# Kernel tuning notes

Measured on AMD Instinct MI355X. Metric: run time of the kernel, lower is better.

Reference implementation:

```python
import jax, jax.numpy as jnp
import numpy as np

N, D, R, E = 50000, 256, 4, 800000
LN_EPS = 1e-5
NEG_INF = -1e30  # finite stand-in for -inf so softmax stays grad-safe


def _layernorm(x, g, b):
    m = x.mean(axis=-1, keepdims=True)
    v = x.var(axis=-1, keepdims=True)
    return (x - m) / jnp.sqrt(v + LN_EPS) * g + b


def setup_inputs() -> dict:
    key = jax.random.key(0)
    ks = jax.random.split(key, 8)
    s = 1.0 / np.sqrt(D).astype(np.float32)
    return {
        'rows': jax.random.randint(ks[0], (R, E), 0, N),
        'cols': jax.random.randint(ks[1], (R, E), 0, N),
        'vals': jax.random.uniform(ks[2], (R, E), jnp.float32),
        'node_emb': jax.random.normal(ks[3], (N, D), jnp.float32) * s,
        'pre_W': jax.random.normal(ks[4], (D, D), jnp.float32) * s,
        'pre_b': jnp.zeros((D,), jnp.float32),
        'ln1_g': jnp.ones((D,), jnp.float32),
        'ln1_b': jnp.zeros((D,), jnp.float32),
        'rel_W': jax.random.normal(ks[5], (R, D, D), jnp.float32) * s,
        'attn_vec': jax.random.normal(ks[6], (D,), jnp.float32) * s,
        'self_W': jax.random.normal(ks[7], (D, D), jnp.float32) * s,
        'self_b': jnp.zeros((D,), jnp.float32),
        'bias': jnp.zeros((D,), jnp.float32),
        'ln2_g': jnp.ones((D,), jnp.float32),
        'ln2_b': jnp.zeros((D,), jnp.float32),
    }


def reference(rows, cols, vals, node_emb, pre_W, pre_b, ln1_g, ln1_b, rel_W,
              attn_vec, self_W, self_b, bias, ln2_g, ln2_b):
    # active_indices = arange(N), so x_all is the full embedding table
    x_all = node_emb
    # pre_encoder: Linear -> LayerNorm -> GELU (exact erf, torch default)
    x = jax.nn.gelu(_layernorm(x_all @ pre_W + pre_b, ln1_g, ln1_b), approximate=False)
    # per-relation: relation linear then SpMM (adj_t @ x_rel) via gather + segment_sum
    msgs = []
    for i in range(R):
        x_rel = x @ rel_W[i]                              # [N, D]
        contrib = vals[i][:, None] * x_rel[cols[i]]       # [E, D]
        msgs.append(jax.ops.segment_sum(contrib, rows[i], num_segments=N))
    stacked = jnp.stack(msgs, axis=1)                     # [N, R, D]
    # semantic attention over relations
    scores = jnp.einsum('nrd,d->nr', stacked, attn_vec)   # [N, R]
    mask = jnp.any(stacked != 0, axis=2)                  # [N, R]
    attn = jax.nn.softmax(jnp.where(mask, scores, NEG_INF), axis=1)
    attn = attn * mask                                    # == nan_to_num(softmax(-inf rows))
    out = jnp.einsum('nrd,nr->nd', stacked, attn) + bias + (x @ self_W + self_b)
    out = jax.nn.gelu(out, approximate=False)
    # active_indices = arange(N): scatter into global index space is identity
    final = _layernorm(out, ln2_g, ln2_b)
    return final, attn, x_all
```

## Files before the change

kernel.cpp:

```cpp
#include <hip/hip_runtime.h>
#include <hip/hip_fp16.h>
#include <math.h>


typedef __attribute__((ext_vector_type(8))) short bf16x8;
typedef __attribute__((ext_vector_type(4))) float f32x4;
typedef __attribute__((ext_vector_type(4))) unsigned u32x4;
typedef unsigned long long u64;

__device__ __forceinline__ float gelu_exact(float v) {
    return 0.5f * v * (1.0f + erff(v * 0.70710678118654752f));
}
__device__ __forceinline__ unsigned short f2bf(float f) {
    unsigned u = __float_as_uint(f);
    return (unsigned short)((u + 0x7fffu + ((u >> 16) & 1u)) >> 16);
}
__device__ __forceinline__ unsigned pack2(float a, float b) {
    return (unsigned)f2bf(a) | ((unsigned)f2bf(b) << 16);
}
__device__ __forceinline__ unsigned short f2h(float f) {
    return __half_as_ushort(__float2half(f));
}
__device__ __forceinline__ __half2 u2h2(unsigned u) {
    union { unsigned u; __half2 h; } c; c.u = u; return c.h;
}
__device__ __forceinline__ void gload16(const void* g, void* l) {
    __builtin_amdgcn_global_load_lds(
        (const __attribute__((address_space(1))) void*)g,
        (__attribute__((address_space(3))) void*)l, 16, 0, 0);
}

__global__ __launch_bounds__(256)
void conv_emb(const float* __restrict__ ne, unsigned short* __restrict__ emb,
              float* __restrict__ outX, int total4)
{
    const int stride = gridDim.x * blockDim.x;
    for (int i = blockIdx.x * blockDim.x + threadIdx.x; i < total4; i += stride) {
        const float4 v = reinterpret_cast<const float4*>(ne)[i];
        reinterpret_cast<float4*>(outX)[i] = v;
        ushort4 h;
        h.x = f2bf(v.x); h.y = f2bf(v.y); h.z = f2bf(v.z); h.w = f2bf(v.w);
        reinterpret_cast<ushort4*>(emb)[i] = h;
    }
}

__global__ __launch_bounds__(256)
void prep_kernel(const float* __restrict__ relW, const float* __restrict__ selfW,
                 const float* __restrict__ preW, const float* __restrict__ av,
                 unsigned short* __restrict__ BTm, unsigned short* __restrict__ BTp,
                 float* __restrict__ wt)
{
    const int blk = blockIdx.x;
    if (blk < 1536) {
        const int idx = blk * 256 + threadIdx.x;
        if (idx < 1280 * 256) {
            const int k = idx >> 8, n = idx & 255;
            const float v = (k < 1024)
                ? relW[(size_t)(k >> 8) * 65536 + (size_t)(k & 255) * 256 + n]
                : selfW[(size_t)(k - 1024) * 256 + n];
            BTm[(size_t)n * 1280 + k] = f2bf(v);
        } else {
            const int i2 = idx - 1280 * 256;
            const int k = i2 >> 8, n = i2 & 255;
            BTp[(size_t)n * 256 + k] = f2bf(preW[(size_t)k * 256 + n]);
        }
    } else {
        __shared__ float avs[256];
        const int r = blk - 1536, tid = threadIdx.x;
        avs[tid] = av[tid];
        __syncthreads();
        const float* W = relW + (size_t)r * 65536 + (size_t)tid * 256;
        float s = 0.f;
        for (int j = 0; j < 256; j += 4) {
            const float4 w4 = *reinterpret_cast<const float4*>(W + j);
            s += w4.x * avs[j] + w4.y * avs[j + 1] + w4.z * avs[j + 2] + w4.w * avs[j + 3];
        }
        wt[r * 256 + tid] = s;
    }
}

template<int MODE>
__global__ __launch_bounds__(512)
void gemm_mfma(const unsigned short* __restrict__ a0,
               const unsigned short* __restrict__ a1,
               const unsigned short* __restrict__ a2,
               const unsigned short* __restrict__ a3,
               const unsigned short* __restrict__ a4,
               const unsigned short* __restrict__ BT,
               const float* __restrict__ bias0, const float* __restrict__ bias1,
               const float* __restrict__ lng, const float* __restrict__ lnb,
               const float* __restrict__ wt, float* __restrict__ Yout,
               float* __restrict__ Cout, unsigned short* __restrict__ XOut,
               unsigned short* __restrict__ XH, int M)
{
    constexpr int K    = MODE ? 1280 : 256;
    constexpr int NSEG = MODE ? 5 : 1;

    __shared__ __align__(16) unsigned char smA[128 * 128];
    __shared__ __align__(16) unsigned char smB[256 * 128];
    __shared__ float redS[4][128];
    __shared__ float redQ[4][128];

    const int tid = threadIdx.x;
    const int w   = tid >> 6;
    const int l   = tid & 63;
    const int wm  = w >> 2, wn = w & 3;
    const int brow = blockIdx.x * 128;

    const int srow = l >> 3;
    const int sgA  = (l & 7) ^ srow;

    f32x4 acc[4][4];
#pragma unroll
    for (int mb = 0; mb < 4; ++mb)
#pragma unroll
        for (int nb = 0; nb < 4; ++nb)
            acc[mb][nb] = f32x4{0.f, 0.f, 0.f, 0.f};

    for (int seg = 0; seg < NSEG; ++seg) {
        const unsigned short* Abase =
            (MODE == 0) ? a0
                        : (seg == 0 ? a0 : seg == 1 ? a1 : seg == 2 ? a2
                                         : seg == 3 ? a3 : a4);
#pragma unroll
        for (int kk = 0; kk < 4; ++kk) {
            __syncthreads();
#pragma unroll
            for (int c = 0; c < 2; ++c) {
                const int r0 = (w * 2 + c) * 8;
                int gm = brow + r0 + srow;
                gm = min(gm, M - 1);
                gload16(Abase + ((size_t)gm << 8) + kk * 64 + sgA * 8,
                        smA + (w * 2 + c) * 1024);
            }
#pragma unroll
            for (int c = 0; c < 4; ++c) {
                const int bn = (w * 4 + c) * 8 + srow;
                gload16(BT + (size_t)bn * K + (seg * 4 + kk) * 64 + sgA * 8,
                        smB + (w * 4 + c) * 1024);
            }
            __syncthreads();

#pragma unroll
            for (int ks = 0; ks < 2; ++ks) {
                bf16x8 af[4], bf[4];
#pragma unroll
                for (int mb = 0; mb < 4; ++mb) {
                    const int row = wm * 64 + mb * 16 + (l & 15);
                    const int g   = (ks * 4 + (l >> 4)) ^ (row & 7);
                    af[mb] = *reinterpret_cast<const bf16x8*>(smA + row * 128 + g * 16);
                }
#pragma unroll
                for (int nb = 0; nb < 4; ++nb) {
                    const int row = wn * 64 + nb * 16 + (l & 15);
                    const int g   = (ks * 4 + (l >> 4)) ^ (row & 7);
                    bf[nb] = *reinterpret_cast<const bf16x8*>(smB + row * 128 + g * 16);
                }
#pragma unroll
                for (int mb = 0; mb < 4; ++mb)
#pragma unroll
                    for (int nb = 0; nb < 4; ++nb)
                        acc[mb][nb] = __builtin_amdgcn_mfma_f32_16x16x32_bf16(
                            af[mb], bf[nb], acc[mb][nb], 0, 0, 0);
            }
        }
    }

    float bb[4], gw[4], bw[4];
#pragma unroll
    for (int nb = 0; nb < 4; ++nb) {
        const int n = wn * 64 + nb * 16 + (l & 15);
        bb[nb] = bias0[n] + (MODE == 1 ? bias1[n] : 0.0f);
        gw[nb] = lng[n];
        bw[nb] = lnb[n];
    }
#pragma unroll
    for (int mb = 0; mb < 4; ++mb)
#pragma unroll
        for (int nb = 0; nb < 4; ++nb)
#pragma unroll
            for (int rg = 0; rg < 4; ++rg) {
                float v = acc[mb][nb][rg] + bb[nb];
                if (MODE == 1) v = gelu_exact(v);
                acc[mb][nb][rg] = v;
            }
#pragma unroll
    for (int mb = 0; mb < 4; ++mb)
#pragma unroll
        for (int rg = 0; rg < 4; ++rg) {
            float s = 0.f, q = 0.f;
#pragma unroll
            for (int nb = 0; nb < 4; ++nb) {
                const float v = acc[mb][nb][rg];
                s += v; q += v * v;
            }
#pragma unroll
            for (int off = 1; off < 16; off <<= 1) {
                s += __shfl_xor(s, off, 64);
                q += __shfl_xor(q, off, 64);
            }
            if ((l & 15) == 0) {
                const int row = wm * 64 + mb * 16 + (l >> 4) * 4 + rg;
                redS[wn][row] = s;
                redQ[wn][row] = q;
            }
        }
    __syncthreads();
    if (tid < 128) {
        const float s = redS[0][tid] + redS[1][tid] + redS[2][tid] + redS[3][tid];
        const float q = redQ[0][tid] + redQ[1][tid] + redQ[2][tid] + redQ[3][tid];
        const float mean = s * (1.0f / 256.0f);
        const float var  = q * (1.0f / 256.0f) - mean * mean;
        redS[0][tid] = mean;
        redQ[0][tid] = rsqrtf(var + 1e-5f);
    }
    __syncthreads();

    float4* yred = reinterpret_cast<float4*>(smA);

#pragma unroll
    for (int mb = 0; mb < 4; ++mb)
#pragma unroll
        for (int rg = 0; rg < 4; ++rg) {
            const int row = wm * 64 + mb * 16 + (l >> 4) * 4 + rg;
            const float mu = redS[0][row];
            const float rs = redQ[0][row];
            const bool rowok = (brow + row < M);
            float yp0 = 0.f, yp1 = 0.f, yp2 = 0.f, yp3 = 0.f;
#pragma unroll
            for (int nb = 0; nb < 4; ++nb) {
                const int n = wn * 64 + nb * 16 + (l & 15);
                const float v = (acc[mb][nb][rg] - mu) * rs * gw[nb] + bw[nb];
                if (MODE == 0) {
                    const float gv = gelu_exact(v);
                    if (rowok) {
                        XOut[((size_t)(brow + row) << 8) + n] = f2bf(gv);
                        XH[((size_t)(brow + row) << 8) + n]   = f2h(gv);
                    }
                    yp0 += gv * wt[n];
                    yp1 += gv * wt[256 + n];
                    yp2 += gv * wt[512 + n];
                    yp3 += gv * wt[768 + n];
                } else {
                    if (rowok) Cout[((size_t)(brow + row) << 8) + n] = v;
                }
            }
            if (MODE == 0) {
#pragma unroll
                for (int off = 1; off < 16; off <<= 1) {
                    yp0 += __shfl_xor(yp0, off, 64);
                    yp1 += __shfl_xor(yp1, off, 64);
                    yp2 += __shfl_xor(yp2, off, 64);
                    yp3 += __shfl_xor(yp3, off, 64);
                }
                if ((l & 15) == 0)
                    yred[wn * 128 + row] = make_float4(yp0, yp1, yp2, yp3);
            }
        }
    if (MODE == 0) {
        __syncthreads();
        if (tid < 128 && brow + tid < M) {
            const float4 a = yred[tid];
            const float4 b = yred[128 + tid];
            const float4 c = yred[256 + tid];
            const float4 d = yred[384 + tid];
            *reinterpret_cast<float4*>(Yout + (size_t)(brow + tid) * 4) =
                make_float4(a.x + b.x + c.x + d.x, a.y + b.y + c.y + d.y,
                            a.z + b.z + c.z + d.z, a.w + b.w + c.w + d.w);
        }
    }
}

__global__ __launch_bounds__(256)
void hist_bin(const int* __restrict__ rows, int* __restrict__ cnt_t,
              int RE, int E, int Nn, int chunk, int NBIN)
{
    __shared__ int lh[800];
    const int blk = blockIdx.x;
    for (int i = threadIdx.x; i < NBIN; i += 256) lh[i] = 0;
    __syncthreads();
    const int e0 = blk * chunk;
    const int e1 = min(e0 + chunk, RE);
    for (int e = e0 + threadIdx.x; e < e1; e += 256) {
        const int r   = e / E;
        const int wid = r * Nn + rows[e];
        atomicAdd(&lh[wid >> 8], 1);
    }
    __syncthreads();
    for (int i = threadIdx.x; i < NBIN; i += 256)
        cnt_t[i * gridDim.x + blk] = lh[i];
}

__global__ __launch_bounds__(256)
void scan_blocks(const int* __restrict__ counts, int* __restrict__ offs,
                 int* __restrict__ bsums, int n)
{
    __shared__ int sh[256];
    const int t = threadIdx.x;
    const int base = blockIdx.x * 1024 + t * 4;
    int v[4], s = 0;
#pragma unroll
    for (int j = 0; j < 4; ++j) {
        v[j] = (base + j < n) ? counts[base + j] : 0;
        s += v[j];
    }
    sh[t] = s;
    __syncthreads();
    for (int off = 1; off < 256; off <<= 1) {
        const int x = (t >= off) ? sh[t - off] : 0;
        __syncthreads();
        sh[t] += x;
        __syncthreads();
    }
    int run = sh[t] - s;
    if (t == 255) bsums[blockIdx.x] = sh[255];
#pragma unroll
    for (int j = 0; j < 4; ++j) {
        if (base + j < n) offs[base + j] = run;
        run += v[j];
    }
}

__global__ __launch_bounds__(256)
void scan_bsums(int* __restrict__ bsums, int nblk)
{
    __shared__ int sh[256];
    const int t = threadIdx.x;
    const int v = (t < nblk) ? bsums[t] : 0;
    sh[t] = v;
    __syncthreads();
    for (int off = 1; off < 256; off <<= 1) {
        const int x = (t >= off) ? sh[t - off] : 0;
        __syncthreads();
        sh[t] += x;
        __syncthreads();
    }
    if (t < nblk) bsums[t] = sh[t] - v;
}

__global__ __launch_bounds__(256)
void scan_add(int* __restrict__ offs, const int* __restrict__ bsums, int n)
{
    const int i = blockIdx.x * 256 + threadIdx.x;
    if (i >= n) return;
    offs[i] += bsums[i >> 10];
}

__global__ __launch_bounds__(256)
void scatter_coarse(const int* __restrict__ rows, const int* __restrict__ cols,
                    const float* __restrict__ vals, const int* __restrict__ ctoffs,
                    u64* __restrict__ edc, int RE, int E, int Nn,
                    int chunk, int NBIN)
{
    __shared__ int lcur[800];
    const int blk = blockIdx.x;
    for (int i = threadIdx.x; i < NBIN; i += 256)
        lcur[i] = ctoffs[i * gridDim.x + blk];
    __syncthreads();
    const int e0 = blk * chunk;
    const int e1 = min(e0 + chunk, RE);
    for (int e = e0 + threadIdx.x; e < e1; e += 256) {
        const int r   = e / E;
        const int row = rows[e];
        const int wid = r * Nn + row;
        const int pos = atomicAdd(&lcur[wid >> 8], 1);
        const unsigned vb = __float_as_uint(vals[e]);
        edc[pos] = ((u64)((vb & 0xFFFFFFFCu) | (unsigned)r) << 32)
                 | ((unsigned)row << 16) | (unsigned)cols[e];
    }
}

__global__ __launch_bounds__(256)
void scatter_fine(const u64* __restrict__ edc, const int* __restrict__ ctoffs,
                  int* __restrict__ offs, unsigned* __restrict__ edata,
                  const float* __restrict__ y, float* __restrict__ SC,
                  int RE, int Nn, int NB1, int NBIN)
{
    __shared__ int   cnt[256];
    __shared__ int   cur[256];
    __shared__ float scr[256];
    const int bin     = blockIdx.x;
    const int widbase = bin << 8;
    const int RN      = Nn << 2;
    const int t       = threadIdx.x;
    cnt[t] = 0;
    scr[t] = 0.f;
    __syncthreads();
    const int cs = ctoffs[bin * NB1];
    const int ce = (bin + 1 < NBIN) ? ctoffs[(bin + 1) * NB1] : RE;
    for (int j = cs + t; j < ce; j += 256) {
        const u64 p = edc[j];
        const unsigned hi = (unsigned)(p >> 32);
        const unsigned lo = (unsigned)p;
        const int w = (int)(hi & 3u) * Nn + (int)(lo >> 16);
        atomicAdd(&cnt[w - widbase], 1);
    }
    __syncthreads();
    const int v = cnt[t];
    cur[t] = v;
    __syncthreads();
    for (int off = 1; off < 256; off <<= 1) {
        const int x = (t >= off) ? cur[t - off] : 0;
        __syncthreads();
        cur[t] += x;
        __syncthreads();
    }
    const int excl = cur[t] - v;
    const int wid  = widbase + t;
    if (wid < RN) offs[wid] = cs + excl;
    __syncthreads();
    cur[t] = cs + excl;
    __syncthreads();
    for (int j = cs + t; j < ce; j += 256) {
        const u64 p  = edc[j];
        const unsigned hi = (unsigned)(p >> 32);
        const unsigned lo = (unsigned)p;
        const int r   = (int)(hi & 3u);
        const int col = (int)(lo & 0xFFFFu);
        const int w   = r * Nn + (int)(lo >> 16);
        const int pos = atomicAdd(&cur[w - widbase], 1);
        const float val = __uint_as_float(hi & 0xFFFFFFFCu);
        edata[pos] = ((unsigned)f2h(val) << 16) | (unsigned)col;
        atomicAdd(&scr[w - widbase], val * y[(size_t)col * 4 + r]);
    }
    __syncthreads();
    if (wid < RN) {
        const int r = wid / Nn;
        const int n = wid - r * Nn;
        SC[(size_t)n * 4 + r] = (v > 0) ? scr[t] : -1e30f;
    }
}

__global__ __launch_bounds__(256)
void softmax4(const float* __restrict__ scores, float* __restrict__ attn, int Nn)
{
    const int n = blockIdx.x * 256 + threadIdx.x;
    if (n >= Nn) return;
    const float4 s4 = *reinterpret_cast<const float4*>(scores + (size_t)n * 4);
    float s[4] = { s4.x, s4.y, s4.z, s4.w };
    float mx = -3.0e38f;
#pragma unroll
    for (int r = 0; r < 4; ++r) mx = fmaxf(mx, s[r]);
    float ex[4], es = 0.f;
#pragma unroll
    for (int r = 0; r < 4; ++r) { ex[r] = expf(s[r] - mx); es += ex[r]; }
    const float inv = 1.0f / es;
    float4 o;
    o.x = (s[0] > -1e29f) ? ex[0] * inv : 0.0f;
    o.y = (s[1] > -1e29f) ? ex[1] * inv : 0.0f;
    o.z = (s[2] > -1e29f) ? ex[2] * inv : 0.0f;
    o.w = (s[3] > -1e29f) ? ex[3] * inv : 0.0f;
    *reinterpret_cast<float4*>(attn + (size_t)n * 4) = o;
}

__global__ __launch_bounds__(256)
void agg_csr(const int* __restrict__ offs, const unsigned* __restrict__ edata,
             const unsigned short* __restrict__ xh, const float* __restrict__ attn,
             unsigned short* __restrict__ agg, int Nn, int RE)
{
    const int wid  = (blockIdx.x << 2) + (threadIdx.x >> 6);
    const int lane = threadIdx.x & 63;
    const int half = lane >> 5;
    const int sub  = lane & 31;
    const int RN   = Nn << 2;
    if (wid >= RN) return;
    const int r = wid / Nn;
    const int n = wid - r * Nn;

    const int start = offs[wid];
    const int end   = (wid + 1 < RN) ? offs[wid + 1] : RE;

    __half2 acc0 = __float2half2_rn(0.f), acc1 = acc0, acc2 = acc0, acc3 = acc0;

    int j = start + half;
    for (; j + 6 < end; j += 8) {
        unsigned e[4];
#pragma unroll
        for (int q = 0; q < 4; ++q)
            e[q] = __builtin_nontemporal_load(edata + j + 2 * q);
        uint4 d[4];
        __half2 vv[4];
#pragma unroll
        for (int q = 0; q < 4; ++q) {
            const int c = (int)(e[q] & 0xFFFFu);
            const __half hv = __ushort_as_half((unsigned short)(e[q] >> 16));
            vv[q] = __half2half2(hv);
            d[q]  = *reinterpret_cast<const uint4*>(xh + ((size_t)c << 8) + sub * 8);
        }
#pragma unroll
        for (int q = 0; q < 4; ++q) {
            acc0 = __hfma2(vv[q], u2h2(d[q].x), acc0);
            acc1 = __hfma2(vv[q], u2h2(d[q].y), acc1);
            acc2 = __hfma2(vv[q], u2h2(d[q].z), acc2);
            acc3 = __hfma2(vv[q], u2h2(d[q].w), acc3);
        }
    }
    for (; j < end; j += 2) {
        const unsigned e0 = __builtin_nontemporal_load(edata + j);
        const int c0 = (int)(e0 & 0xFFFFu);
        const __half hv = __ushort_as_half((unsigned short)(e0 >> 16));
        const __half2 v0 = __half2half2(hv);
        const uint4 d0 = *reinterpret_cast<const uint4*>(xh + ((size_t)c0 << 8) + sub * 8);
        acc0 = __hfma2(v0, u2h2(d0.x), acc0);
        acc1 = __hfma2(v0, u2h2(d0.y), acc1);
        acc2 = __hfma2(v0, u2h2(d0.z), acc2);
        acc3 = __hfma2(v0, u2h2(d0.w), acc3);
    }

    float a[8];
    a[0] = __low2float(acc0); a[1] = __high2float(acc0);
    a[2] = __low2float(acc1); a[3] = __high2float(acc1);
    a[4] = __low2float(acc2); a[5] = __high2float(acc2);
    a[6] = __low2float(acc3); a[7] = __high2float(acc3);
#pragma unroll
    for (int i = 0; i < 8; ++i) a[i] += __shfl_xor(a[i], 32, 64);

    if (half == 0) {
        const float sc = attn[(size_t)n * 4 + r];
        u32x4 st;
        st.x = pack2(sc * a[0], sc * a[1]);
        st.y = pack2(sc * a[2], sc * a[3]);
        st.z = pack2(sc * a[4], sc * a[5]);
        st.w = pack2(sc * a[6], sc * a[7]);
        __builtin_nontemporal_store(
            st, reinterpret_cast<u32x4*>(agg + ((size_t)wid << 8) + sub * 8));
    }
}

extern "C" void kernel_launch(void* const* d_in, const int* in_sizes, int n_in,
                              void* d_out, int out_size, void* d_ws, size_t ws_size,
                              hipStream_t stream)
{
    const int*   rows     = (const int*)d_in[0];
    const int*   cols     = (const int*)d_in[1];
    const float* vals     = (const float*)d_in[2];
    const float* node_emb = (const float*)d_in[3];
    const float* pre_W    = (const float*)d_in[4];
    const float* pre_b    = (const float*)d_in[5];
    const float* ln1_g    = (const float*)d_in[6];
    const float* ln1_b    = (const float*)d_in[7];
    const float* rel_W    = (const float*)d_in[8];
    const float* attn_vec = (const float*)d_in[9];
    const float* self_W   = (const float*)d_in[10];
    const float* self_b   = (const float*)d_in[11];
    const float* bias     = (const float*)d_in[12];
    const float* ln2_g    = (const float*)d_in[13];
    const float* ln2_b    = (const float*)d_in[14];

    const int Dd = 256;
    const int R  = in_sizes[8] / (Dd * Dd);
    const int N  = in_sizes[3] / Dd;
    const int E  = in_sizes[0] / R;
    const int RE = R * E;
    const int RN = R * N;

    const int NB1   = 256;
    const int chunk = (RE + NB1 - 1) / NB1;
    const int NBIN  = (RN + 255) / 256;
    const int NCT   = NBIN * NB1;

    float* out  = (float*)d_out;
    float* outF = out;
    float* outA = out + (size_t)N * Dd;
    float* outX = outA + (size_t)N * R;

    char* wp = (char*)d_ws;
    auto alloc = [&](size_t bytes) {
        char* p = wp;
        wp += (bytes + 255) & ~(size_t)255;
        return p;
    };
    unsigned short* AGGS = (unsigned short*)alloc((size_t)RN * Dd * 2);
    unsigned short* XB   = (unsigned short*)alloc((size_t)N * Dd * 2);
    unsigned short* XH   = (unsigned short*)alloc((size_t)N * Dd * 2);
    unsigned short* EMB  = (unsigned short*)alloc((size_t)N * Dd * 2);
    unsigned short* BTm  = (unsigned short*)alloc((size_t)Dd * 1280 * 2);
    unsigned short* BTp  = (unsigned short*)alloc((size_t)Dd * Dd * 2);
    float* WT   = (float*)alloc((size_t)R * Dd * 4);
    float* Y    = (float*)alloc((size_t)N * R * 4);
    float* SC   = (float*)alloc((size_t)N * R * 4);
    int* offs   = (int*)alloc((size_t)RN * 4);
    int* cnt_t  = (int*)alloc((size_t)NCT * 4);
    int* ctoffs = cnt_t;
    int* bsums2 = (int*)alloc(1024);
    unsigned* edata = (unsigned*)alloc((size_t)RE * 4);
    u64* edc    = (u64*)alloc((size_t)RE * 8);

    const int gblocks = (N + 127) / 128;
    const int nblkC   = (NCT + 1023) / 1024;

    prep_kernel<<<1540, 256, 0, stream>>>(rel_W, self_W, pre_W, attn_vec,
                                          BTm, BTp, WT);
    conv_emb<<<2048, 256, 0, stream>>>(node_emb, EMB, outX, N * Dd / 4);

    gemm_mfma<0><<<gblocks, 512, 0, stream>>>(EMB, nullptr, nullptr, nullptr, nullptr,
                                              BTp, pre_b, nullptr, ln1_g, ln1_b,
                                              WT, Y, nullptr, XB, XH, N);

    hist_bin<<<NB1, 256, 0, stream>>>(rows, cnt_t, RE, E, N, chunk, NBIN);
    scan_blocks<<<nblkC, 256, 0, stream>>>(cnt_t, ctoffs, bsums2, NCT);
    scan_bsums<<<1, 256, 0, stream>>>(bsums2, nblkC);
    scan_add<<<(NCT + 255) / 256, 256, 0, stream>>>(ctoffs, bsums2, NCT);
    scatter_coarse<<<NB1, 256, 0, stream>>>(rows, cols, vals, ctoffs, edc,
                                            RE, E, N, chunk, NBIN);
    scatter_fine<<<NBIN, 256, 0, stream>>>(edc, ctoffs, offs, edata, Y, SC,
                                           RE, N, NB1, NBIN);

    softmax4<<<(N + 255) / 256, 256, 0, stream>>>(SC, outA, N);

    agg_csr<<<(RN + 3) / 4, 256, 0, stream>>>(offs, edata, XH, outA, AGGS, N, RE);

    gemm_mfma<1><<<gblocks, 512, 0, stream>>>(AGGS, AGGS + (size_t)N * Dd,
                                              AGGS + (size_t)2 * N * Dd,
                                              AGGS + (size_t)3 * N * Dd, XB,
                                              BTm, bias, self_b, ln2_g, ln2_b,
                                              nullptr, nullptr,
                                              outF, nullptr, nullptr, N);
}
```

Measured before the change: 539.4 us.

## Fuse sparse aggregation into final GEMM and switch MFMA to fp16

Removes the separate agg_csr kernel and the AGGS intermediate by having each GEMM block gather its 128 rows' neighbor sums per relation directly into a 512-byte-wide LDS A tile, then run the MFMA over all five K segments. All GEMM operands switch from bf16 to fp16, so the separate bf16 copy of X is no longer needed and the fp16 XH buffer feeds both the aggregation and the self term. This saves the write and reread of a large aggregated tensor and one launch. The cost is that gather latency now sits serially inside the GEMM block with only about 390 blocks, lower occupancy from 64KB+ of LDS, and fp16 range risk.

Measured after the change: 719.5 us. 33.4% more time.

```diff
diff --git a/kernel.cpp b/kernel.cpp
--- a/kernel.cpp
+++ b/kernel.cpp
@@ -3,7 +3,7 @@
 #include <math.h>
 
 
-typedef __attribute__((ext_vector_type(8))) short bf16x8;
+typedef __attribute__((ext_vector_type(8))) _Float16 f16x8;
 typedef __attribute__((ext_vector_type(4))) float f32x4;
 typedef __attribute__((ext_vector_type(4))) unsigned u32x4;
 typedef unsigned long long u64;
@@ -11,15 +11,11 @@
 __device__ __forceinline__ float gelu_exact(float v) {
     return 0.5f * v * (1.0f + erff(v * 0.70710678118654752f));
 }
-__device__ __forceinline__ unsigned short f2bf(float f) {
-    unsigned u = __float_as_uint(f);
-    return (unsigned short)((u + 0x7fffu + ((u >> 16) & 1u)) >> 16);
-}
-__device__ __forceinline__ unsigned pack2(float a, float b) {
-    return (unsigned)f2bf(a) | ((unsigned)f2bf(b) << 16);
-}
 __device__ __forceinline__ unsigned short f2h(float f) {
     return __half_as_ushort(__float2half(f));
+}
+__device__ __forceinline__ unsigned pack2h(float a, float b) {
+    return (unsigned)f2h(a) | ((unsigned)f2h(b) << 16);
 }
 __device__ __forceinline__ __half2 u2h2(unsigned u) {
     union { unsigned u; __half2 h; } c; c.u = u; return c.h;
@@ -39,7 +35,7 @@
         const float4 v = reinterpret_cast<const float4*>(ne)[i];
         reinterpret_cast<float4*>(outX)[i] = v;
         ushort4 h;
-        h.x = f2bf(v.x); h.y = f2bf(v.y); h.z = f2bf(v.z); h.w = f2bf(v.w);
+        h.x = f2h(v.x); h.y = f2h(v.y); h.z = f2h(v.z); h.w = f2h(v.w);
         reinterpret_cast<ushort4*>(emb)[i] = h;
     }
 }
@@ -58,11 +54,11 @@
             const float v = (k < 1024)
                 ? relW[(size_t)(k >> 8) * 65536 + (size_t)(k & 255) * 256 + n]
                 : selfW[(size_t)(k - 1024) * 256 + n];
-            BTm[(size_t)n * 1280 + k] = f2bf(v);
+            BTm[(size_t)n * 1280 + k] = f2h(v);
         } else {
             const int i2 = idx - 1280 * 256;
             const int k = i2 >> 8, n = i2 & 255;
-            BTp[(size_t)n * 256 + k] = f2bf(preW[(size_t)k * 256 + n]);
+            BTp[(size_t)n * 256 + k] = f2h(preW[(size_t)k * 256 + n]);
         }
     } else {
         __shared__ float avs[256];
@@ -79,23 +75,13 @@
     }
 }
 
-template<int MODE>
 __global__ __launch_bounds__(512)
-void gemm_mfma(const unsigned short* __restrict__ a0,
-               const unsigned short* __restrict__ a1,
-               const unsigned short* __restrict__ a2,
-               const unsigned short* __restrict__ a3,
-               const unsigned short* __restrict__ a4,
-               const unsigned short* __restrict__ BT,
-               const float* __restrict__ bias0, const float* __restrict__ bias1,
-               const float* __restrict__ lng, const float* __restrict__ lnb,
-               const float* __restrict__ wt, float* __restrict__ Yout,
-               float* __restrict__ Cout, unsigned short* __restrict__ XOut,
-               unsigned short* __restrict__ XH, int M)
-{
-    constexpr int K    = MODE ? 1280 : 256;
-    constexpr int NSEG = MODE ? 5 : 1;
-
+void gemm_pre(const unsigned short* __restrict__ A,
+              const unsigned short* __restrict__ BT,
+              const float* __restrict__ bias0, const float* __restrict__ lng,
+              const float* __restrict__ lnb, const float* __restrict__ wt,
+              float* __restrict__ Yout, unsigned short* __restrict__ XH, int M)
+{
     __shared__ __align__(16) unsigned char smA[128 * 128];
     __shared__ __align__(16) unsigned char smB[256 * 128];
     __shared__ float redS[4][128];
@@ -108,7 +94,7 @@
     const int brow = blockIdx.x * 128;
 
     const int srow = l >> 3;
-    const int sgA  = (l & 7) ^ srow;
+    const int sg   = (l & 7) ^ srow;
 
     f32x4 acc[4][4];
 #pragma unroll
@@ -117,52 +103,45 @@
         for (int nb = 0; nb < 4; ++nb)
             acc[mb][nb] = f32x4{0.f, 0.f, 0.f, 0.f};
 
-    for (int seg = 0; seg < NSEG; ++seg) {
-        const unsigned short* Abase =
-            (MODE == 0) ? a0
-                        : (seg == 0 ? a0 : seg == 1 ? a1 : seg == 2 ? a2
-                                         : seg == 3 ? a3 : a4);
-#pragma unroll
-        for (int kk = 0; kk < 4; ++kk) {
-            __syncthreads();
-#pragma unroll
-            for (int c = 0; c < 2; ++c) {
-                const int r0 = (w * 2 + c) * 8;
-                int gm = brow + r0 + srow;
-                gm = min(gm, M - 1);
-                gload16(Abase + ((size_t)gm << 8) + kk * 64 + sgA * 8,
-                        smA + (w * 2 + c) * 1024);
-            }
-#pragma unroll
-            for (int c = 0; c < 4; ++c) {
-                const int bn = (w * 4 + c) * 8 + srow;
-                gload16(BT + (size_t)bn * K + (seg * 4 + kk) * 64 + sgA * 8,
-                        smB + (w * 4 + c) * 1024);
-            }
-            __syncthreads();
-
-#pragma unroll
-            for (int ks = 0; ks < 2; ++ks) {
-                bf16x8 af[4], bf[4];
-#pragma unroll
-                for (int mb = 0; mb < 4; ++mb) {
-                    const int row = wm * 64 + mb * 16 + (l & 15);
-                    const int g   = (ks * 4 + (l >> 4)) ^ (row & 7);
-                    af[mb] = *reinterpret_cast<const bf16x8*>(smA + row * 128 + g * 16);
-                }
-#pragma unroll
-                for (int nb = 0; nb < 4; ++nb) {
-                    const int row = wn * 64 + nb * 16 + (l & 15);
-                    const int g   = (ks * 4 + (l >> 4)) ^ (row & 7);
-                    bf[nb] = *reinterpret_cast<const bf16x8*>(smB + row * 128 + g * 16);
-                }
-#pragma unroll
-                for (int mb = 0; mb < 4; ++mb)
-#pragma unroll
-                    for (int nb = 0; nb < 4; ++nb)
-                        acc[mb][nb] = __builtin_amdgcn_mfma_f32_16x16x32_bf16(
-                            af[mb], bf[nb], acc[mb][nb], 0, 0, 0);
-            }
+#pragma unroll
+    for (int kk = 0; kk < 4; ++kk) {
+        __syncthreads();
+#pragma unroll
+        for (int c = 0; c < 2; ++c) {
+            int gm = brow + (w * 2 + c) * 8 + srow;
+            gm = min(gm, M - 1);
+            gload16(A + ((size_t)gm << 8) + kk * 64 + sg * 8,
+                    smA + (w * 2 + c) * 1024);
+        }
+#pragma unroll
+        for (int c = 0; c < 4; ++c) {
+            const int bn = (w * 4 + c) * 8 + srow;
+            gload16(BT + (size_t)bn * 256 + kk * 64 + sg * 8,
+                    smB + (w * 4 + c) * 1024);
+        }
+        __syncthreads();
+
+#pragma unroll
+        for (int ks = 0; ks < 2; ++ks) {
+            f16x8 af[4], bf[4];
+#pragma unroll
+            for (int mb = 0; mb < 4; ++mb) {
+                const int row = wm * 64 + mb * 16 + (l & 15);
+                const int g   = (ks * 4 + (l >> 4)) ^ (row & 7);
+                af[mb] = *reinterpret_cast<const f16x8*>(smA + row * 128 + g * 16);
+            }
+#pragma unroll
+            for (int nb = 0; nb < 4; ++nb) {
+                const int row = wn * 64 + nb * 16 + (l & 15);
+                const int g   = (ks * 4 + (l >> 4)) ^ (row & 7);
+                bf[nb] = *reinterpret_cast<const f16x8*>(smB + row * 128 + g * 16);
+            }
+#pragma unroll
+            for (int mb = 0; mb < 4; ++mb)
+#pragma unroll
+                for (int nb = 0; nb < 4; ++nb)
+                    acc[mb][nb] = __builtin_amdgcn_mfma_f32_16x16x32_f16(
+                        af[mb], bf[nb], acc[mb][nb], 0, 0, 0);
         }
     }
 
@@ -170,7 +149,7 @@
 #pragma unroll
     for (int nb = 0; nb < 4; ++nb) {
         const int n = wn * 64 + nb * 16 + (l & 15);
-        bb[nb] = bias0[n] + (MODE == 1 ? bias1[n] : 0.0f);
+        bb[nb] = bias0[n];
         gw[nb] = lng[n];
         bw[nb] = lnb[n];
     }
@@ -179,11 +158,8 @@
 #pragma unroll
         for (int nb = 0; nb < 4; ++nb)
 #pragma unroll
-            for (int rg = 0; rg < 4; ++rg) {
-                float v = acc[mb][nb][rg] + bb[nb];
-                if (MODE == 1) v = gelu_exact(v);
-                acc[mb][nb][rg] = v;
-            }
+            for (int rg = 0; rg < 4; ++rg) acc[mb][nb][rg] += bb[nb];
+
 #pragma unroll
     for (int mb = 0; mb < 4; ++mb)
 #pragma unroll
@@ -230,44 +206,33 @@
 #pragma unroll
             for (int nb = 0; nb < 4; ++nb) {
                 const int n = wn * 64 + nb * 16 + (l & 15);
-                const float v = (acc[mb][nb][rg] - mu) * rs * gw[nb] + bw[nb];
-                if (MODE == 0) {
-                    const float gv = gelu_exact(v);
-                    if (rowok) {
-                        XOut[((size_t)(brow + row) << 8) + n] = f2bf(gv);
-                        XH[((size_t)(brow + row) << 8) + n]   = f2h(gv);
-                    }
-                    yp0 += gv * wt[n];
-                    yp1 += gv * wt[256 + n];
-                    yp2 += gv * wt[512 + n];
-                    yp3 += gv * wt[768 + n];
-                } else {
-                    if (rowok) Cout[((size_t)(brow + row) << 8) + n] = v;
-                }
-            }
-            if (MODE == 0) {
-#pragma unroll
-                for (int off = 1; off < 16; off <<= 1) {
-                    yp0 += __shfl_xor(yp0, off, 64);
-                    yp1 += __shfl_xor(yp1, off, 64);
-                    yp2 += __shfl_xor(yp2, off, 64);
-                    yp3 += __shfl_xor(yp3, off, 64);
-                }
-                if ((l & 15) == 0)
-                    yred[wn * 128 + row] = make_float4(yp0, yp1, yp2, yp3);
-            }
-        }
-    if (MODE == 0) {
-        __syncthreads();
-        if (tid < 128 && brow + tid < M) {
-            const float4 a = yred[tid];
-            const float4 b = yred[128 + tid];
-            const float4 c = yred[256 + tid];
-            const float4 d = yred[384 + tid];
-            *reinterpret_cast<float4*>(Yout + (size_t)(brow + tid) * 4) =
-                make_float4(a.x + b.x + c.x + d.x, a.y + b.y + c.y + d.y,
-                            a.z + b.z + c.z + d.z, a.w + b.w + c.w + d.w);
-        }
+                const float v  = (acc[mb][nb][rg] - mu) * rs * gw[nb] + bw[nb];
+                const float gv = gelu_exact(v);
+                if (rowok) XH[((size_t)(brow + row) << 8) + n] = f2h(gv);
+                yp0 += gv * wt[n];
+                yp1 += gv * wt[256 + n];
+                yp2 += gv * wt[512 + n];
+                yp3 += gv * wt[768 + n];
+            }
+#pragma unroll
+            for (int off = 1; off < 16; off <<= 1) {
+                yp0 += __shfl_xor(yp0, off, 64);
+                yp1 += __shfl_xor(yp1, off, 64);
+                yp2 += __shfl_xor(yp2, off, 64);
+                yp3 += __shfl_xor(yp3, off, 64);
+            }
+            if ((l & 15) == 0)
+                yred[wn * 128 + row] = make_float4(yp0, yp1, yp2, yp3);
+        }
+    __syncthreads();
+    if (tid < 128 && brow + tid < M) {
+        const float4 a = yred[tid];
+        const float4 b = yred[128 + tid];
+        const float4 c = yred[256 + tid];
+        const float4 d = yred[384 + tid];
+        *reinterpret_cast<float4*>(Yout + (size_t)(brow + tid) * 4) =
+            make_float4(a.x + b.x + c.x + d.x, a.y + b.y + c.y + d.y,
+                        a.z + b.z + c.z + d.z, a.w + b.w + c.w + d.w);
     }
 }
 
@@ -453,78 +418,212 @@
     *reinterpret_cast<float4*>(attn + (size_t)n * 4) = o;
 }
 
-__global__ __launch_bounds__(256)
-void agg_csr(const int* __restrict__ offs, const unsigned* __restrict__ edata,
-             const unsigned short* __restrict__ xh, const float* __restrict__ attn,
-             unsigned short* __restrict__ agg, int Nn, int RE)
-{
-    const int wid  = (blockIdx.x << 2) + (threadIdx.x >> 6);
-    const int lane = threadIdx.x & 63;
-    const int half = lane >> 5;
-    const int sub  = lane & 31;
+__global__ __launch_bounds__(512)
+void gemm_fused1(const int* __restrict__ offs, const unsigned* __restrict__ edata,
+                 const unsigned short* __restrict__ xh,
+                 const float* __restrict__ attn,
+                 const unsigned short* __restrict__ BT,
+                 const float* __restrict__ bias0, const float* __restrict__ bias1,
+                 const float* __restrict__ lng, const float* __restrict__ lnb,
+                 float* __restrict__ Cout, int M, int Nn, int RE)
+{
+    __shared__ __align__(16) unsigned char smA[128 * 512];
+    __shared__ __align__(16) unsigned char smB[256 * 128];
+    __shared__ float redS[4][128];
+    __shared__ float redQ[4][128];
+
+    const int tid  = threadIdx.x;
+    const int w    = tid >> 6;
+    const int l    = tid & 63;
+    const int wm   = w >> 2, wn = w & 3;
+    const int brow = blockIdx.x * 128;
+    const int half = l >> 5;
+    const int sub  = l & 31;
     const int RN   = Nn << 2;
-    if (wid >= RN) return;
-    const int r = wid / Nn;
-    const int n = wid - r * Nn;
-
-    const int start = offs[wid];
-    const int end   = (wid + 1 < RN) ? offs[wid + 1] : RE;
-
-    __half2 acc0 = __float2half2_rn(0.f), acc1 = acc0, acc2 = acc0, acc3 = acc0;
-
-    int j = start + half;
-    for (; j + 6 < end; j += 8) {
-        unsigned e[4];
-#pragma unroll
-        for (int q = 0; q < 4; ++q)
-            e[q] = __builtin_nontemporal_load(edata + j + 2 * q);
-        uint4 d[4];
-        __half2 vv[4];
-#pragma unroll
-        for (int q = 0; q < 4; ++q) {
-            const int c = (int)(e[q] & 0xFFFFu);
-            const __half hv = __ushort_as_half((unsigned short)(e[q] >> 16));
-            vv[q] = __half2half2(hv);
-            d[q]  = *reinterpret_cast<const uint4*>(xh + ((size_t)c << 8) + sub * 8);
-        }
-#pragma unroll
-        for (int q = 0; q < 4; ++q) {
-            acc0 = __hfma2(vv[q], u2h2(d[q].x), acc0);
-            acc1 = __hfma2(vv[q], u2h2(d[q].y), acc1);
-            acc2 = __hfma2(vv[q], u2h2(d[q].z), acc2);
-            acc3 = __hfma2(vv[q], u2h2(d[q].w), acc3);
-        }
-    }
-    for (; j < end; j += 2) {
-        const unsigned e0 = __builtin_nontemporal_load(edata + j);
-        const int c0 = (int)(e0 & 0xFFFFu);
-        const __half hv = __ushort_as_half((unsigned short)(e0 >> 16));
-        const __half2 v0 = __half2half2(hv);
-        const uint4 d0 = *reinterpret_cast<const uint4*>(xh + ((size_t)c0 << 8) + sub * 8);
-        acc0 = __hfma2(v0, u2h2(d0.x), acc0);
-        acc1 = __hfma2(v0, u2h2(d0.y), acc1);
-        acc2 = __hfma2(v0, u2h2(d0.z), acc2);
-        acc3 = __hfma2(v0, u2h2(d0.w), acc3);
-    }
-
-    float a[8];
-    a[0] = __low2float(acc0); a[1] = __high2float(acc0);
-    a[2] = __low2float(acc1); a[3] = __high2float(acc1);
-    a[4] = __low2float(acc2); a[5] = __high2float(acc2);
-    a[6] = __low2float(acc3); a[7] = __high2float(acc3);
-#pragma unroll
-    for (int i = 0; i < 8; ++i) a[i] += __shfl_xor(a[i], 32, 64);
-
-    if (half == 0) {
-        const float sc = attn[(size_t)n * 4 + r];
-        u32x4 st;
-        st.x = pack2(sc * a[0], sc * a[1]);
-        st.y = pack2(sc * a[2], sc * a[3]);
-        st.z = pack2(sc * a[4], sc * a[5]);
-        st.w = pack2(sc * a[6], sc * a[7]);
-        __builtin_nontemporal_store(
-            st, reinterpret_cast<u32x4*>(agg + ((size_t)wid << 8) + sub * 8));
-    }
+
+    const int srow = l >> 3;
+    const int sgB  = (l & 7) ^ srow;
+
+    f32x4 acc[4][4];
+#pragma unroll
+    for (int mb = 0; mb < 4; ++mb)
+#pragma unroll
+        for (int nb = 0; nb < 4; ++nb)
+            acc[mb][nb] = f32x4{0.f, 0.f, 0.f, 0.f};
+
+    for (int seg = 0; seg < 5; ++seg) {
+        __syncthreads();
+        if (seg < 4) {
+            const int nbase = brow + w * 16;
+            const int wbase = seg * Nn + nbase;
+            const int oval = offs[min(wbase + min(l, 16), RN - 1)];
+            for (int nn = 0; nn < 16; ++nn) {
+                const int row  = w * 16 + nn;
+                const int node = brow + row;
+                int start = 0, end = 0;
+                if (node < Nn) {
+                    const int wid = wbase + nn;
+                    start = __shfl(oval, nn, 64);
+                    end   = (wid < RN - 1) ? __shfl(oval, nn + 1, 64) : RE;
+                }
+                __half2 h0 = __float2half2_rn(0.f), h1 = h0, h2 = h0, h3 = h0;
+                int j = start + half;
+                for (; j + 6 < end; j += 8) {
+                    unsigned e[4];
+#pragma unroll
+                    for (int q = 0; q < 4; ++q)
+                        e[q] = __builtin_nontemporal_load(edata + j + 2 * q);
+                    uint4 d[4];
+                    __half2 vv[4];
+#pragma unroll
+                    for (int q = 0; q < 4; ++q) {
+                        const int c = (int)(e[q] & 0xFFFFu);
+                        vv[q] = __half2half2(__ushort_as_half((unsigned short)(e[q] >> 16)));
+                        d[q]  = *reinterpret_cast<const uint4*>(xh + ((size_t)c << 8) + sub * 8);
+                    }
+#pragma unroll
+                    for (int q = 0; q < 4; ++q) {
+                        h0 = __hfma2(vv[q], u2h2(d[q].x), h0);
+                        h1 = __hfma2(vv[q], u2h2(d[q].y), h1);
+                        h2 = __hfma2(vv[q], u2h2(d[q].z), h2);
+                        h3 = __hfma2(vv[q], u2h2(d[q].w), h3);
+                    }
+                }
+                for (; j < end; j += 2) {
+                    const unsigned e0 = __builtin_nontemporal_load(edata + j);
+                    const int c0 = (int)(e0 & 0xFFFFu);
+                    const __half2 v0 = __half2half2(__ushort_as_half((unsigned short)(e0 >> 16)));
+                    const uint4 d0 = *reinterpret_cast<const uint4*>(xh + ((size_t)c0 << 8) + sub * 8);
+                    h0 = __hfma2(v0, u2h2(d0.x), h0);
+                    h1 = __hfma2(v0, u2h2(d0.y), h1);
+                    h2 = __hfma2(v0, u2h2(d0.z), h2);
+                    h3 = __hfma2(v0, u2h2(d0.w), h3);
+                }
+                float a[8];
+                a[0] = __low2float(h0); a[1] = __high2float(h0);
+                a[2] = __low2float(h1); a[3] = __high2float(h1);
+                a[4] = __low2float(h2); a[5] = __high2float(h2);
+                a[6] = __low2float(h3); a[7] = __high2float(h3);
+#pragma unroll
+                for (int i = 0; i < 8; ++i) a[i] += __shfl_xor(a[i], 32, 64);
+                const float sc = (node < Nn) ? attn[(size_t)node * 4 + seg] : 0.0f;
+                if (half == 0) {
+                    u32x4 st;
+                    st.x = pack2h(sc * a[0], sc * a[1]);
+                    st.y = pack2h(sc * a[2], sc * a[3]);
+                    st.z = pack2h(sc * a[4], sc * a[5]);
+                    st.w = pack2h(sc * a[6], sc * a[7]);
+                    *reinterpret_cast<u32x4*>(
+                        smA + row * 512 + ((sub ^ (row & 7)) << 4)) = st;
+                }
+            }
+        } else {
+#pragma unroll
+            for (int c = 0; c < 8; ++c) {
+                const int r0  = (w * 8 + c) * 2;
+                const int row = r0 + (l >> 5);
+                const int gm  = min(brow + row, M - 1);
+                gload16(xh + ((size_t)gm << 8) + ((sub ^ (row & 7)) * 8),
+                        smA + r0 * 512);
+            }
+        }
+        for (int kk = 0; kk < 4; ++kk) {
+            __syncthreads();
+#pragma unroll
+            for (int c = 0; c < 4; ++c) {
+                const int bn = (w * 4 + c) * 8 + srow;
+                gload16(BT + (size_t)bn * 1280 + (seg * 4 + kk) * 64 + sgB * 8,
+                        smB + (w * 4 + c) * 1024);
+            }
+            __syncthreads();
+
+#pragma unroll
+            for (int ks = 0; ks < 2; ++ks) {
+                f16x8 af[4], bf[4];
+#pragma unroll
+                for (int mb = 0; mb < 4; ++mb) {
+                    const int row = wm * 64 + mb * 16 + (l & 15);
+                    const int g   = (kk * 8 + ks * 4 + (l >> 4)) ^ (row & 7);
+                    af[mb] = *reinterpret_cast<const f16x8*>(smA + row * 512 + g * 16);
+                }
+#pragma unroll
+                for (int nb = 0; nb < 4; ++nb) {
+                    const int row = wn * 64 + nb * 16 + (l & 15);
+                    const int g   = (ks * 4 + (l >> 4)) ^ (row & 7);
+                    bf[nb] = *reinterpret_cast<const f16x8*>(smB + row * 128 + g * 16);
+                }
+#pragma unroll
+                for (int mb = 0; mb < 4; ++mb)
+#pragma unroll
+                    for (int nb = 0; nb < 4; ++nb)
+                        acc[mb][nb] = __builtin_amdgcn_mfma_f32_16x16x32_f16(
+                            af[mb], bf[nb], acc[mb][nb], 0, 0, 0);
+            }
+        }
+    }
+
+    float bb[4], gw[4], bw[4];
+#pragma unroll
+    for (int nb = 0; nb < 4; ++nb) {
+        const int n = wn * 64 + nb * 16 + (l & 15);
+        bb[nb] = bias0[n] + bias1[n];
+        gw[nb] = lng[n];
+        bw[nb] = lnb[n];
+    }
+#pragma unroll
+    for (int mb = 0; mb < 4; ++mb)
+#pragma unroll
+        for (int nb = 0; nb < 4; ++nb)
+#pragma unroll
+            for (int rg = 0; rg < 4; ++rg)
+                acc[mb][nb][rg] = gelu_exact(acc[mb][nb][rg] + bb[nb]);
+
+#pragma unroll
+    for (int mb = 0; mb < 4; ++mb)
+#pragma unroll
+        for (int rg = 0; rg < 4; ++rg) {
+            float s = 0.f, q = 0.f;
+#pragma unroll
+            for (int nb = 0; nb < 4; ++nb) {
+                const float v = acc[mb][nb][rg];
+                s += v; q += v * v;
+            }
+#pragma unroll
+            for (int off = 1; off < 16; off <<= 1) {
+                s += __shfl_xor(s, off, 64);
+                q += __shfl_xor(q, off, 64);
+            }
+            if ((l & 15) == 0) {
+                const int row = wm * 64 + mb * 16 + (l >> 4) * 4 + rg;
+                redS[wn][row] = s;
+                redQ[wn][row] = q;
+            }
+        }
+    __syncthreads();
+    if (tid < 128) {
+        const float s = redS[0][tid] + redS[1][tid] + redS[2][tid] + redS[3][tid];
+        const float q = redQ[0][tid] + redQ[1][tid] + redQ[2][tid] + redQ[3][tid];
+        const float mean = s * (1.0f / 256.0f);
+        const float var  = q * (1.0f / 256.0f) - mean * mean;
+        redS[0][tid] = mean;
+        redQ[0][tid] = rsqrtf(var + 1e-5f);
+    }
+    __syncthreads();
+#pragma unroll
+    for (int mb = 0; mb < 4; ++mb)
+#pragma unroll
+        for (int rg = 0; rg < 4; ++rg) {
+            const int row = wm * 64 + mb * 16 + (l >> 4) * 4 + rg;
+            if (brow + row >= M) continue;
+            const float mu = redS[0][row];
+            const float rs = redQ[0][row];
+#pragma unroll
+            for (int nb = 0; nb < 4; ++nb) {
+                const int n = wn * 64 + nb * 16 + (l & 15);
+                Cout[((size_t)(brow + row) << 8) + n] =
+                    (acc[mb][nb][rg] - mu) * rs * gw[nb] + bw[nb];
+            }
+        }
 }
 
 extern "C" void kernel_launch(void* const* d_in, const int* in_sizes, int n_in,
@@ -570,16 +669,14 @@
         wp += (bytes + 255) & ~(size_t)255;
         return p;
     };
-    unsigned short* AGGS = (unsigned short*)alloc((size_t)RN * Dd * 2);
-    unsigned short* XB   = (unsigned short*)alloc((size_t)N * Dd * 2);
-    unsigned short* XH   = (unsigned short*)alloc((size_t)N * Dd * 2);
-    unsigned short* EMB  = (unsigned short*)alloc((size_t)N * Dd * 2);
-    unsigned short* BTm  = (unsigned short*)alloc((size_t)Dd * 1280 * 2);
-    unsigned short* BTp  = (unsigned short*)alloc((size_t)Dd * Dd * 2);
+    unsigned short* XH  = (unsigned short*)alloc((size_t)N * Dd * 2);
+    unsigned short* EMB = (unsigned short*)alloc((size_t)N * Dd * 2);
+    unsigned short* BTm = (unsigned short*)alloc((size_t)Dd * 1280 * 2);
+    unsigned short* BTp = (unsigned short*)alloc((size_t)Dd * Dd * 2);
     float* WT   = (float*)alloc((size_t)R * Dd * 4);
     float* Y    = (float*)alloc((size_t)N * R * 4);
     float* SC   = (float*)alloc((size_t)N * R * 4);
-    int* offs   = (int*)alloc((size_t)RN * 4);
+    int* offs   = (int*)alloc((size_t)(RN + 1) * 4);
     int* cnt_t  = (int*)alloc((size_t)NCT * 4);
     int* ctoffs = cnt_t;
     int* bsums2 = (int*)alloc(1024);
@@ -593,9 +690,8 @@
                                           BTm, BTp, WT);
     conv_emb<<<2048, 256, 0, stream>>>(node_emb, EMB, outX, N * Dd / 4);
 
-    gemm_mfma<0><<<gblocks, 512, 0, stream>>>(EMB, nullptr, nullptr, nullptr, nullptr,
-                                              BTp, pre_b, nullptr, ln1_g, ln1_b,
-                                              WT, Y, nullptr, XB, XH, N);
+    gemm_pre<<<gblocks, 512, 0, stream>>>(EMB, BTp, pre_b, ln1_g, ln1_b,
+                                          WT, Y, XH, N);
 
     hist_bin<<<NB1, 256, 0, stream>>>(rows, cnt_t, RE, E, N, chunk, NBIN);
     scan_blocks<<<nblkC, 256, 0, stream>>>(cnt_t, ctoffs, bsums2, NCT);
@@ -608,12 +704,7 @@
 
     softmax4<<<(N + 255) / 256, 256, 0, stream>>>(SC, outA, N);
 
-    agg_csr<<<(RN + 3) / 4, 256, 0, stream>>>(offs, edata, XH, outA, AGGS, N, RE);
-
-    gemm_mfma<1><<<gblocks, 512, 0, stream>>>(AGGS, AGGS + (size_t)N * Dd,
-                                              AGGS + (size_t)2 * N * Dd,
-                                              AGGS + (size_t)3 * N * Dd, XB,
-                                              BTm, bias, self_b, ln2_g, ln2_b,
-                                              nullptr, nullptr,
-                                              outF, nullptr, nullptr, N);
-}
+    gemm_fused1<<<gblocks, 512, 0, stream>>>(offs, edata, XH, outA, BTm,
+                                             bias, self_b, ln2_g, ln2_b,
+                                             outF, N, N, RE);
+}
```
